# Optimization experiments

Measured on AMD Instinct MI355X. Metric: run time of the kernel, lower is better.

## Reference

```python
import jax, jax.numpy as jnp
import numpy as np

NUM_ITERS = 20

def setup_inputs() -> dict:
    key = jax.random.key(0)
    log_alpha = jax.random.normal(key, (2048, 256, 256), dtype=jnp.float32)
    return {"log_alpha": log_alpha}

def reference(log_alpha) -> jnp.ndarray:
    in_dtype = log_alpha.dtype
    P0 = log_alpha.astype(jnp.float32)

    def body(P, _):
        # row normalization (logsumexp over last dim), then column normalization
        P = P - jax.scipy.special.logsumexp(P, axis=-1, keepdims=True)
        P = P - jax.scipy.special.logsumexp(P, axis=-2, keepdims=True)
        return P, None

    P, _ = jax.lax.scan(body, P0, None, length=NUM_ITERS)
    return jnp.exp(P).astype(in_dtype)
```

## Files before the change

### kernel.cpp

```cpp
#include <hip/hip_runtime.h>

typedef _Float16 h2 __attribute__((ext_vector_type(2)));
typedef _Float16 h4 __attribute__((ext_vector_type(4)));
typedef float f4 __attribute__((ext_vector_type(4)));

#define MAT_N 256
#define MAT_ELEMS (MAT_N * MAT_N)
#define NUM_ITERS 20

template<int CTRL>
__device__ __forceinline__ float dpp_add(float x) {
    int i = __builtin_bit_cast(int, x);
    int r = __builtin_amdgcn_update_dpp(i, i, CTRL, 0xF, 0xF, true);
    return x + __builtin_bit_cast(float, r);
}
__device__ __forceinline__ float row16_reduce(float x) {
    x = dpp_add<0xB1>(x);
    x = dpp_add<0x4E>(x);
    x = dpp_add<0x141>(x);
    x = dpp_add<0x140>(x);
    return x;
}

__device__ __forceinline__ float dot2(h2 a, h2 b, float c) {
    return __builtin_amdgcn_fdot2(a, b, c, false);
}
__device__ __forceinline__ h2 pkrtz(float a, float b) {
    return __builtin_bit_cast(h2, __builtin_amdgcn_cvt_pkrtz(a, b));
}

__global__ __launch_bounds__(512, 2) void sinkhorn_kernel(
        const float* __restrict__ in, float* __restrict__ out) {
    const int tid = threadIdx.x;
    const int C = tid & 15;
    const int R = tid >> 4;

    __shared__ __align__(16) h2 Q1h[32][130];
    __shared__ __align__(16) h2 Vch[128];

    if (blockIdx.x < 512 && ((blockIdx.x >> 3) & 1)) {
        __builtin_amdgcn_s_sleep(127);
        __builtin_amdgcn_s_sleep(127);
    }

    const size_t base = (size_t)blockIdx.x * MAT_ELEMS;
    const f4* __restrict__ in4 = (const f4*)(in + base);
    f4* __restrict__ out4 = (f4*)(out + base);

    h2 qp[8][8];
    #pragma unroll
    for (int i = 0; i < 8; ++i) {
        #pragma unroll
        for (int d = 0; d < 4; ++d) {
            f4 t = in4[(8 * R + i) * 64 + C + 16 * d];
            h2 a, b;
            a.x = (_Float16)__expf(t.x); a.y = (_Float16)__expf(t.y);
            b.x = (_Float16)__expf(t.z); b.y = (_Float16)__expf(t.w);
            qp[i][2 * d] = a; qp[i][2 * d + 1] = b;
        }
    }

    h2 vp[8];
    {
        h2 one; one.x = (_Float16)1.f; one.y = (_Float16)1.f;
        #pragma unroll
        for (int j = 0; j < 8; ++j) vp[j] = one;
    }
    float u[8];

    #pragma unroll 1
    for (int it = 0; it < NUM_ITERS; ++it) {
        #pragma unroll
        for (int i = 0; i < 8; ++i) {
            float s = dot2(qp[i][0], vp[0], 0.f);
            #pragma unroll
            for (int jj = 1; jj < 8; ++jj) s = dot2(qp[i][jj], vp[jj], s);
            s = row16_reduce(s);
            u[i] = __builtin_amdgcn_rcpf(s);
        }

        h2 ca[8];
        {
            h2 z; z.x = (_Float16)0.f; z.y = (_Float16)0.f;
            #pragma unroll
            for (int p = 0; p < 8; ++p) ca[p] = z;
        }
        #pragma unroll
        for (int i = 0; i < 8; ++i) {
            const h2 ub = pkrtz(u[i], u[i]);
            #pragma unroll
            for (int p = 0; p < 8; ++p)
                ca[p] = __builtin_elementwise_fma(qp[i][p], ub, ca[p]);
        }

        #pragma unroll
        for (int d = 0; d < 4; ++d) {
            h4 wv;
            wv.x = ca[2 * d].x;     wv.y = ca[2 * d].y;
            wv.z = ca[2 * d + 1].x; wv.w = ca[2 * d + 1].y;
            *(h4*)&Q1h[R][2 * C + 32 * d] = wv;
        }
        __syncthreads();

        {
            const int cp = tid >> 2;
            const int r0 = (tid & 3) * 8;
            h2 p0 = Q1h[r0 + 0][cp] + Q1h[r0 + 1][cp];
            h2 p1 = Q1h[r0 + 2][cp] + Q1h[r0 + 3][cp];
            h2 p2 = Q1h[r0 + 4][cp] + Q1h[r0 + 5][cp];
            h2 p3 = Q1h[r0 + 6][cp] + Q1h[r0 + 7][cp];
            float lo = ((float)p0.x + (float)p1.x) + ((float)p2.x + (float)p3.x);
            float hi = ((float)p0.y + (float)p1.y) + ((float)p2.y + (float)p3.y);
            lo = dpp_add<0xB1>(lo); lo = dpp_add<0x4E>(lo);
            hi = dpp_add<0xB1>(hi); hi = dpp_add<0x4E>(hi);
            if ((tid & 3) == 0) {
                Vch[cp] = pkrtz(__builtin_amdgcn_rcpf(lo),
                                __builtin_amdgcn_rcpf(hi));
            }
        }
        __syncthreads();

        #pragma unroll
        for (int d = 0; d < 4; ++d) {
            h4 t = *(const h4*)&Vch[2 * C + 32 * d];
            h2 t0, t1;
            t0.x = t.x; t0.y = t.y; t1.x = t.z; t1.y = t.w;
            vp[2 * d] = t0; vp[2 * d + 1] = t1;
        }
    }

    float vf[16];
    #pragma unroll
    for (int p = 0; p < 8; ++p) {
        vf[2 * p]     = (float)vp[p].x;
        vf[2 * p + 1] = (float)vp[p].y;
    }
    #pragma unroll
    for (int i = 0; i < 8; ++i) {
        const float s = u[i];
        #pragma unroll
        for (int d = 0; d < 4; ++d) {
            f4 o;
            o.x = (float)qp[i][2 * d].x     * (s * vf[4 * d]);
            o.y = (float)qp[i][2 * d].y     * (s * vf[4 * d + 1]);
            o.z = (float)qp[i][2 * d + 1].x * (s * vf[4 * d + 2]);
            o.w = (float)qp[i][2 * d + 1].y * (s * vf[4 * d + 3]);
            __builtin_nontemporal_store(o, &out4[(8 * R + i) * 64 + C + 16 * d]);
        }
    }
}

extern "C" void kernel_launch(void* const* d_in, const int* in_sizes, int n_in,
                              void* d_out, int out_size, void* d_ws, size_t ws_size,
                              hipStream_t stream) {
    const float* in = (const float*)d_in[0];
    float* out = (float*)d_out;
    const int nmat = in_sizes[0] / MAT_ELEMS;
    sinkhorn_kernel<<<nmat, 512, 0, stream>>>(in, out);
}
```

Baseline: 244.6 us.

## Process four matrices per persistent block and interleave next-matrix loads with output stores

Each block now handles four consecutive matrices instead of one, shrinking the grid by four. During the output phase of one matrix it loads and exponentiates the next matrix's rows into the same registers, so global reads overlap with the nontemporal stores. The staggered-sleep trick now applies to all blocks. The cost is less parallelism across blocks (512 blocks total) and more work serialized inside each block, which can hurt load balance and latency hiding. It also assumes nmat is divisible by MPB.

```diff
diff --git a/kernel.cpp b/kernel.cpp
--- a/kernel.cpp
+++ b/kernel.cpp
@@ -7,6 +7,7 @@
 #define MAT_N 256
 #define MAT_ELEMS (MAT_N * MAT_N)
 #define NUM_ITERS 20
+#define MPB 4
 
 template<int CTRL>
 __device__ __forceinline__ float dpp_add(float x) {
@@ -30,7 +31,7 @@
 }
 
 __global__ __launch_bounds__(512, 2) void sinkhorn_kernel(
-        const float* __restrict__ in, float* __restrict__ out) {
+        const float* __restrict__ in, float* __restrict__ out, int nmat) {
     const int tid = threadIdx.x;
     const int C = tid & 15;
     const int R = tid >> 4;
@@ -38,114 +39,137 @@
     __shared__ __align__(16) h2 Q1h[32][130];
     __shared__ __align__(16) h2 Vch[128];
 
-    if (blockIdx.x < 512 && ((blockIdx.x >> 3) & 1)) {
+    if ((blockIdx.x >> 3) & 1) {
         __builtin_amdgcn_s_sleep(127);
         __builtin_amdgcn_s_sleep(127);
     }
 
-    const size_t base = (size_t)blockIdx.x * MAT_ELEMS;
-    const f4* __restrict__ in4 = (const f4*)(in + base);
-    f4* __restrict__ out4 = (f4*)(out + base);
+    const int m0 = blockIdx.x * MPB;
 
     h2 qp[8][8];
-    #pragma unroll
-    for (int i = 0; i < 8; ++i) {
+    {
+        const f4* __restrict__ in4 = (const f4*)(in + (size_t)m0 * MAT_ELEMS);
         #pragma unroll
-        for (int d = 0; d < 4; ++d) {
-            f4 t = in4[(8 * R + i) * 64 + C + 16 * d];
-            h2 a, b;
-            a.x = (_Float16)__expf(t.x); a.y = (_Float16)__expf(t.y);
-            b.x = (_Float16)__expf(t.z); b.y = (_Float16)__expf(t.w);
-            qp[i][2 * d] = a; qp[i][2 * d + 1] = b;
+        for (int i = 0; i < 8; ++i) {
+            #pragma unroll
+            for (int d = 0; d < 4; ++d) {
+                f4 t = in4[(8 * R + i) * 64 + C + 16 * d];
+                h2 a, b;
+                a.x = (_Float16)__expf(t.x); a.y = (_Float16)__expf(t.y);
+                b.x = (_Float16)__expf(t.z); b.y = (_Float16)__expf(t.w);
+                qp[i][2 * d] = a; qp[i][2 * d + 1] = b;
+            }
         }
     }
 
-    h2 vp[8];
-    {
-        h2 one; one.x = (_Float16)1.f; one.y = (_Float16)1.f;
-        #pragma unroll
-        for (int j = 0; j < 8; ++j) vp[j] = one;
-    }
-    float u[8];
+    #pragma unroll 1
+    for (int mi = 0; mi < MPB; ++mi) {
+        h2 vp[8];
+        {
+            h2 one; one.x = (_Float16)1.f; one.y = (_Float16)1.f;
+            #pragma unroll
+            for (int j = 0; j < 8; ++j) vp[j] = one;
+        }
+        float u[8];
 
-    #pragma unroll 1
-    for (int it = 0; it < NUM_ITERS; ++it) {
-        #pragma unroll
-        for (int i = 0; i < 8; ++i) {
-            float s = dot2(qp[i][0], vp[0], 0.f);
+        #pragma unroll 1
+        for (int it = 0; it < NUM_ITERS; ++it) {
             #pragma unroll
-            for (int jj = 1; jj < 8; ++jj) s = dot2(qp[i][jj], vp[jj], s);
-            s = row16_reduce(s);
-            u[i] = __builtin_amdgcn_rcpf(s);
+            for (int i = 0; i < 8; ++i) {
+                float s = dot2(qp[i][0], vp[0], 0.f);
+                #pragma unroll
+                for (int jj = 1; jj < 8; ++jj) s = dot2(qp[i][jj], vp[jj], s);
+                s = row16_reduce(s);
+                u[i] = __builtin_amdgcn_rcpf(s);
+            }
+
+            h2 ca[8];
+            {
+                h2 z; z.x = (_Float16)0.f; z.y = (_Float16)0.f;
+                #pragma unroll
+                for (int p = 0; p < 8; ++p) ca[p] = z;
+            }
+            #pragma unroll
+            for (int i = 0; i < 8; ++i) {
+                const h2 ub = pkrtz(u[i], u[i]);
+                #pragma unroll
+                for (int p = 0; p < 8; ++p)
+                    ca[p] = __builtin_elementwise_fma(qp[i][p], ub, ca[p]);
+            }
+            #pragma unroll
+            for (int d = 0; d < 4; ++d) {
+                h4 wv;
+                wv.x = ca[2 * d].x;     wv.y = ca[2 * d].y;
+                wv.z = ca[2 * d + 1].x; wv.w = ca[2 * d + 1].y;
+                *(h4*)&Q1h[R][2 * C + 32 * d] = wv;
+            }
+            __syncthreads();
+
+            {
+                const int cp = tid >> 2;
+                const int r0 = (tid & 3) * 8;
+                h2 p0 = Q1h[r0 + 0][cp] + Q1h[r0 + 1][cp];
+                h2 p1 = Q1h[r0 + 2][cp] + Q1h[r0 + 3][cp];
+                h2 p2 = Q1h[r0 + 4][cp] + Q1h[r0 + 5][cp];
+                h2 p3 = Q1h[r0 + 6][cp] + Q1h[r0 + 7][cp];
+                float lo = ((float)p0.x + (float)p1.x) + ((float)p2.x + (float)p3.x);
+                float hi = ((float)p0.y + (float)p1.y) + ((float)p2.y + (float)p3.y);
+                lo = dpp_add<0xB1>(lo); lo = dpp_add<0x4E>(lo);
+                hi = dpp_add<0xB1>(hi); hi = dpp_add<0x4E>(hi);
+                if ((tid & 3) == 0) {
+                    Vch[cp] = pkrtz(__builtin_amdgcn_rcpf(lo),
+                                    __builtin_amdgcn_rcpf(hi));
+                }
+            }
+            __syncthreads();
+
+            #pragma unroll
+            for (int d = 0; d < 4; ++d) {
+                h4 t = *(const h4*)&Vch[2 * C + 32 * d];
+                h2 t0, t1;
+                t0.x = t.x; t0.y = t.y; t1.x = t.z; t1.y = t.w;
+                vp[2 * d] = t0; vp[2 * d + 1] = t1;
+            }
         }
 
-        h2 ca[8];
-        {
-            h2 z; z.x = (_Float16)0.f; z.y = (_Float16)0.f;
-            #pragma unroll
-            for (int p = 0; p < 8; ++p) ca[p] = z;
+        const bool last = (mi == MPB - 1);
+        const f4* __restrict__ nin4 =
+            (const f4*)(in + (size_t)(m0 + mi + 1) * MAT_ELEMS);
+        f4* __restrict__ out4 = (f4*)(out + (size_t)(m0 + mi) * MAT_ELEMS);
+
+        float vf[16];
+        #pragma unroll
+        for (int p = 0; p < 8; ++p) {
+            vf[2 * p]     = (float)vp[p].x;
+            vf[2 * p + 1] = (float)vp[p].y;
         }
         #pragma unroll
         for (int i = 0; i < 8; ++i) {
-            const h2 ub = pkrtz(u[i], u[i]);
+            f4 tnew[4];
+            if (!last) {
+                #pragma unroll
+                for (int d = 0; d < 4; ++d)
+                    tnew[d] = nin4[(8 * R + i) * 64 + C + 16 * d];
+            }
+            const float s = u[i];
             #pragma unroll
-            for (int p = 0; p < 8; ++p)
-                ca[p] = __builtin_elementwise_fma(qp[i][p], ub, ca[p]);
-        }
-
-        #pragma unroll
-        for (int d = 0; d < 4; ++d) {
-            h4 wv;
-            wv.x = ca[2 * d].x;     wv.y = ca[2 * d].y;
-            wv.z = ca[2 * d + 1].x; wv.w = ca[2 * d + 1].y;
-            *(h4*)&Q1h[R][2 * C + 32 * d] = wv;
-        }
-        __syncthreads();
-
-        {
-            const int cp = tid >> 2;
-            const int r0 = (tid & 3) * 8;
-            h2 p0 = Q1h[r0 + 0][cp] + Q1h[r0 + 1][cp];
-            h2 p1 = Q1h[r0 + 2][cp] + Q1h[r0 + 3][cp];
-            h2 p2 = Q1h[r0 + 4][cp] + Q1h[r0 + 5][cp];
-            h2 p3 = Q1h[r0 + 6][cp] + Q1h[r0 + 7][cp];
-            float lo = ((float)p0.x + (float)p1.x) + ((float)p2.x + (float)p3.x);
-            float hi = ((float)p0.y + (float)p1.y) + ((float)p2.y + (float)p3.y);
-            lo = dpp_add<0xB1>(lo); lo = dpp_add<0x4E>(lo);
-            hi = dpp_add<0xB1>(hi); hi = dpp_add<0x4E>(hi);
-            if ((tid & 3) == 0) {
-                Vch[cp] = pkrtz(__builtin_amdgcn_rcpf(lo),
-                                __builtin_amdgcn_rcpf(hi));
+            for (int d = 0; d < 4; ++d) {
+                f4 o;
+                o.x = (float)qp[i][2 * d].x     * (s * vf[4 * d]);
+                o.y = (float)qp[i][2 * d].y     * (s * vf[4 * d + 1]);
+                o.z = (float)qp[i][2 * d + 1].x * (s * vf[4 * d + 2]);
+                o.w = (float)qp[i][2 * d + 1].y * (s * vf[4 * d + 3]);
+                __builtin_nontemporal_store(o, &out4[(8 * R + i) * 64 + C + 16 * d]);
             }
-        }
-        __syncthreads();
-
-        #pragma unroll
-        for (int d = 0; d < 4; ++d) {
-            h4 t = *(const h4*)&Vch[2 * C + 32 * d];
-            h2 t0, t1;
-            t0.x = t.x; t0.y = t.y; t1.x = t.z; t1.y = t.w;
-            vp[2 * d] = t0; vp[2 * d + 1] = t1;
-        }
-    }
-
-    float vf[16];
-    #pragma unroll
-    for (int p = 0; p < 8; ++p) {
-        vf[2 * p]     = (float)vp[p].x;
-        vf[2 * p + 1] = (float)vp[p].y;
-    }
-    #pragma unroll
-    for (int i = 0; i < 8; ++i) {
-        const float s = u[i];
-        #pragma unroll
-        for (int d = 0; d < 4; ++d) {
-            f4 o;
-            o.x = (float)qp[i][2 * d].x     * (s * vf[4 * d]);
-            o.y = (float)qp[i][2 * d].y     * (s * vf[4 * d + 1]);
-            o.z = (float)qp[i][2 * d + 1].x * (s * vf[4 * d + 2]);
-            o.w = (float)qp[i][2 * d + 1].y * (s * vf[4 * d + 3]);
-            __builtin_nontemporal_store(o, &out4[(8 * R + i) * 64 + C + 16 * d]);
+            if (!last) {
+                #pragma unroll
+                for (int d = 0; d < 4; ++d) {
+                    h2 a, b;
+                    a.x = (_Float16)__expf(tnew[d].x); a.y = (_Float16)__expf(tnew[d].y);
+                    b.x = (_Float16)__expf(tnew[d].z); b.y = (_Float16)__expf(tnew[d].w);
+                    qp[i][2 * d] = a; qp[i][2 * d + 1] = b;
+                }
+            }
         }
     }
 }
@@ -156,5 +180,6 @@
     const float* in = (const float*)d_in[0];
     float* out = (float*)d_out;
     const int nmat = in_sizes[0] / MAT_ELEMS;
-    sinkhorn_kernel<<<nmat, 512, 0, stream>>>(in, out);
+    const int grid = nmat / MPB;
+    sinkhorn_kernel<<<grid, 512, 0, stream>>>(in, out, nmat);
 }
```

Result: slower. 338.1 us (+38.2%).
